# Kernel optimization log

Hardware: AMD Instinct MI355X
Metric: run time of the kernel (lower is better)

The kernel has to match this reference:

```python
import jax, jax.numpy as jnp
import numpy as np

N = 38332        # nodes = poi_len - 1 (pinned by fc_layer in_features)
POI_LEN = 38333
CAT_LEN = 400
POI_DIM = 300
CAT_DIM = 100
C = 128          # gcn_channel
L = 5            # gcn_layers
E = 1200000      # edges
NEG = 0.01       # nn.LeakyReLU default slope
GAT_NEG = 0.2    # GATConv attention slope


def _leaky(x, s=NEG):
    return jnp.where(x > 0, x, s * x)


def _gcn_conv(x, W, b, src, dst, ew):
    # PyG GCNConv: self-loops already appended in (src,dst,ew); symmetric norm
    xw = x @ W
    deg = jax.ops.segment_sum(ew, dst, num_segments=N)
    dinv = jnp.where(deg > 0, jax.lax.rsqrt(deg), 0.0)
    norm = dinv[src] * ew * dinv[dst]
    out = jax.ops.segment_sum(xw[src] * norm[:, None], dst, num_segments=N)
    return out + b


def _gat_conv(x, W, a_src, a_dst, b, src, dst):
    # PyG GATConv, 1 head; self-loops already in (src,dst)
    xw = x @ W                      # [N, C]
    al = xw @ a_src                 # [N]
    ar = xw @ a_dst                 # [N]
    e = _leaky(al[src] + ar[dst], GAT_NEG)          # [E+N]
    emax = jax.ops.segment_max(e, dst, num_segments=N)
    ex = jnp.exp(e - emax[dst])
    denom = jax.ops.segment_sum(ex, dst, num_segments=N)
    att = ex / denom[dst]
    out = jax.ops.segment_sum(xw[src] * att[:, None], dst, num_segments=N)
    return out + b


def _graph_norm(x, gamma, beta, alpha, eps=1e-5):
    # PyG GraphNorm over the single graph (all nodes)
    mean = x.mean(0)
    xc = x - alpha * mean
    var = (xc * xc).mean(0)
    return gamma * xc * jax.lax.rsqrt(var + eps) + beta


def _forward(poi_ids, cat_ids, feat3, edge_index, edge_weight, poi_emb, cat_emb,
             Win, b_in, gcn_W, gcn_b, gn_gamma, gn_beta, gn_alpha,
             gat_W, gat_asrc, gat_adst, gat_b, Wout, b_out,
             fc_W1, fc_b1, fc_W2, fc_b2):
    loops = jnp.arange(N, dtype=edge_index.dtype)
    src = jnp.concatenate([edge_index[0], loops])
    dst = jnp.concatenate([edge_index[1], loops])
    ew = jnp.concatenate([edge_weight, jnp.ones((N,), edge_weight.dtype)])
    # node features: [poi_emb | cat_emb | 3 raw floats] -> [N, 403]
    feat = jnp.concatenate([poi_emb[poi_ids], cat_emb[cat_ids], feat3], axis=1)
    x = _leaky(_gcn_conv(feat, Win, b_in, src, dst, ew))
    for l in range(L):  # GcnUnit stack (shared GraphNorm within a unit)
        t = _leaky(_graph_norm(_gcn_conv(x, gcn_W[l], gcn_b[l], src, dst, ew),
                               gn_gamma[l], gn_beta[l], gn_alpha[l]))
        x = x + t
        t = _leaky(_graph_norm(_gat_conv(x, gat_W[l], gat_asrc[l], gat_adst[l], gat_b[l], src, dst),
                               gn_gamma[l], gn_beta[l], gn_alpha[l]))
        x = x + t
    x = _leaky(_gcn_conv(x, Wout, b_out, src, dst, ew)).reshape(-1)  # [N]
    h = jax.nn.relu(x @ fc_W1 + fc_b1)
    return jax.nn.relu(h @ fc_W2 + fc_b2)  # [POI_LEN]


def setup_inputs() -> dict:
    key = jax.random.key(0)
    ks = iter(jax.random.split(key, 24))
    nrm = lambda s, sc=0.05: jax.random.normal(next(ks), s, dtype=jnp.float32) * sc
    return {
        'poi_ids': jax.random.randint(next(ks), (N,), 0, POI_LEN),
        'cat_ids': jax.random.randint(next(ks), (N,), 0, CAT_LEN),
        'feat3': jax.random.normal(next(ks), (N, 3), dtype=jnp.float32),
        'edge_index': jax.random.randint(next(ks), (2, E), 0, N),
        'edge_weight': jax.random.uniform(next(ks), (E,), dtype=jnp.float32),
        'poi_emb': nrm((POI_LEN, POI_DIM)),
        'cat_emb': nrm((CAT_LEN, CAT_DIM)),
        'Win': nrm((POI_DIM + CAT_DIM + 3, C)),
        'b_in': jnp.zeros((C,), jnp.float32),
        'gcn_W': nrm((L, C, C)),
        'gcn_b': jnp.zeros((L, C), jnp.float32),
        'gn_gamma': jnp.ones((L, C), jnp.float32),
        'gn_beta': jnp.zeros((L, C), jnp.float32),
        'gn_alpha': jnp.ones((L, C), jnp.float32),
        'gat_W': nrm((L, C, C)),
        'gat_asrc': nrm((L, C)),
        'gat_adst': nrm((L, C)),
        'gat_b': jnp.zeros((L, C), jnp.float32),
        'Wout': nrm((C, 1)),
        'b_out': jnp.zeros((1,), jnp.float32),
        'fc_W1': nrm((N, 128)),
        'fc_b1': jnp.zeros((128,), jnp.float32),
        'fc_W2': nrm((128, POI_LEN)),
        'fc_b2': jnp.zeros((POI_LEN,), jnp.float32),
    }


def reference(poi_ids, cat_ids, feat3, edge_index, edge_weight, poi_emb, cat_emb,
              Win, b_in, gcn_W, gcn_b, gn_gamma, gn_beta, gn_alpha,
              gat_W, gat_asrc, gat_adst, gat_b, Wout, b_out,
              fc_W1, fc_b1, fc_W2, fc_b2):
    return _forward(poi_ids, cat_ids, feat3, edge_index, edge_weight, poi_emb, cat_emb,
                    Win, b_in, gcn_W, gcn_b, gn_gamma, gn_beta, gn_alpha,
                    gat_W, gat_asrc, gat_adst, gat_b, Wout, b_out,
                    fc_W1, fc_b1, fc_W2, fc_b2)
```

## Files before the change

kernel.cpp:

```cpp
#include <hip/hip_runtime.h>

typedef unsigned short ushort_t;
typedef __attribute__((ext_vector_type(8))) short short8v;
typedef __attribute__((ext_vector_type(4))) float floatx4;

__device__ __forceinline__ float b2f(ushort_t u) {
    unsigned int x = ((unsigned int)u) << 16;
    float f; __builtin_memcpy(&f, &x, 4); return f;
}
__device__ __forceinline__ ushort_t f2b(float f) {
    unsigned int x; __builtin_memcpy(&x, &f, 4);
    unsigned int lsb = (x >> 16) & 1u;
    x += 0x7fffu + lsb;
    return (ushort_t)(x >> 16);
}
__device__ __forceinline__ float leaky01(float v) { return v > 0.f ? v : 0.01f * v; }

__global__ void init_k(int* cnt, int N) {
    int i = blockIdx.x * 256 + threadIdx.x;
    if (i < N) cnt[i] = 1;
}

__global__ void count_k(const int* __restrict__ ei, int* cnt, int* pos, int E) {
    int e = blockIdx.x * 256 + threadIdx.x;
    if (e < E) pos[e] = atomicAdd(&cnt[ei[E + e]], 1);
}

__launch_bounds__(1024)
__global__ void scan_k(const int* __restrict__ cnt, int* rp, int n) {
    __shared__ int wsum[16];
    int tid = threadIdx.x; int lane = tid & 63, wid = tid >> 6;
    int base = 0;
    for (int start = 0; start < n; start += 4096) {
        int v[4]; int s = 0;
        #pragma unroll
        for (int j = 0; j < 4; ++j) {
            int i = start + tid * 4 + j;
            v[j] = (i < n) ? cnt[i] : 0; s += v[j];
        }
        int sc = s;
        #pragma unroll
        for (int off = 1; off < 64; off <<= 1) {
            int t = __shfl_up(sc, off);
            if (lane >= off) sc += t;
        }
        if (lane == 63) wsum[wid] = sc;
        __syncthreads();
        if (wid == 0) {
            int ws = (lane < 16) ? wsum[lane] : 0;
            #pragma unroll
            for (int off = 1; off < 16; off <<= 1) {
                int t = __shfl_up(ws, off);
                if (lane >= off) ws += t;
            }
            if (lane < 16) wsum[lane] = ws;
        }
        __syncthreads();
        int wbase = (wid > 0) ? wsum[wid - 1] : 0;
        int excl = base + wbase + (sc - s);
        #pragma unroll
        for (int j = 0; j < 4; ++j) {
            int i = start + tid * 4 + j;
            if (i < n) rp[i] = excl;
            excl += v[j];
        }
        int total = wsum[15];
        __syncthreads();
        base += total;
    }
    if (tid == 0) rp[n] = base;
}

__global__ void post_k(const int* __restrict__ rp, float2* er, int N) {
    int i = blockIdx.x * 256 + threadIdx.x;
    if (i < N) er[rp[i]] = make_float2(__int_as_float(i), 1.0f);
}

__global__ void scat_k(const int* __restrict__ ei, const float* __restrict__ ew,
                       const int* __restrict__ rp, const int* __restrict__ pos,
                       float2* er, int E) {
    int e = blockIdx.x * 256 + threadIdx.x;
    if (e < E) {
        int dst = ei[E + e];
        er[rp[dst] + pos[e]] = make_float2(__int_as_float(ei[e]), ew[e]);
    }
}

__global__ void deg_k(const int* __restrict__ rp, const float2* __restrict__ er,
                      float* dinv, int N) {
    int wave = threadIdx.x >> 6, lane = threadIdx.x & 63;
    int node = blockIdx.x * 4 + wave;
    if (node >= N) return;
    int s0 = rp[node], end = rp[node + 1];
    float sum = 0.f;
    for (int s = s0 + lane; s < end; s += 64) sum += er[s].y;
    #pragma unroll
    for (int off = 32; off; off >>= 1) sum += __shfl_xor(sum, off);
    if (lane == 0) dinv[node] = rsqrtf(sum);
}

__global__ void coef_k(const int* __restrict__ rp, float2* er,
                       const float* __restrict__ dinv, int N) {
    int wave = threadIdx.x >> 6, lane = threadIdx.x & 63;
    int node = blockIdx.x * 4 + wave;
    if (node >= N) return;
    int s0 = rp[node], end = rp[node + 1];
    float dn = dinv[node];
    for (int s = s0 + lane; s < end; s += 64) {
        float2 r = er[s];
        int src = __float_as_int(r.x);
        r.y = dinv[src] * r.y * dn;
        er[s] = r;
    }
}

__global__ void prep_w(const float* __restrict__ gcn_W, const float* __restrict__ gat_W,
                       const float* __restrict__ Win, ushort_t* __restrict__ wt,
                       ushort_t* __restrict__ wtin) {
    int idx = blockIdx.x * 256 + threadIdx.x;
    if (idx < 10 * 16384) {
        int l = idx >> 14, r = idx & 16383;
        int n = r >> 7, k = r & 127;
        const float* src = (l < 5) ? (gcn_W + l * 16384) : (gat_W + (l - 5) * 16384);
        wt[idx] = f2b(src[k * 128 + n]);
    } else {
        int idx2 = idx - 10 * 16384;
        if (idx2 < 128 * 320) {
            int n = idx2 / 320, k = idx2 - n * 320;
            wtin[idx2] = f2b(k < 300 ? Win[k * 128 + n] : 0.f);
        }
    }
}

__global__ void cat_proj_k(const float* __restrict__ ce, const float* __restrict__ Win,
                           float* __restrict__ cp) {
    __shared__ float row[100];
    int r = blockIdx.x, tid = threadIdx.x;
    if (tid < 100) row[tid] = ce[r * 100 + tid];
    __syncthreads();
    float acc = 0.f;
    #pragma unroll 4
    for (int k = 0; k < 100; ++k) acc += row[k] * Win[(300 + k) * 128 + tid];
    cp[r * 128 + tid] = acc;
}

__launch_bounds__(256)
__global__ void poi_gemm(const float* __restrict__ pe, const ushort_t* __restrict__ wtin,
                         ushort_t* __restrict__ pp, int P) {
    __shared__ __align__(16) ushort_t As[64 * 328];
    int tid = threadIdx.x;
    int wid = tid >> 6, lane = tid & 63;
    int r0 = blockIdx.x * 64;
    #pragma unroll
    for (int p = 0; p < 19; ++p) {
        int idx = tid + p * 256;
        if (idx < 4800) {
            int row = idx / 75, kq = idx - row * 75;
            int grow = r0 + row;
            float4 v = make_float4(0.f, 0.f, 0.f, 0.f);
            if (grow < P) v = *(const float4*)&pe[(size_t)grow * 300 + kq * 4];
            ushort4 b;
            b.x = f2b(v.x); b.y = f2b(v.y); b.z = f2b(v.z); b.w = f2b(v.w);
            *(ushort4*)&As[row * 328 + kq * 4] = b;
        }
    }
    #pragma unroll
    for (int p = 0; p < 5; ++p) {
        int idx = tid + p * 256;
        if (idx < 1280) {
            int row = idx / 20, j = idx - row * 20;
            As[row * 328 + 300 + j] = 0;
        }
    }
    __syncthreads();
    int m = lane & 15, q = lane >> 4;
    short8v af[10];
    #pragma unroll
    for (int kc = 0; kc < 10; ++kc)
        af[kc] = *(const short8v*)&As[(wid * 16 + m) * 328 + kc * 32 + q * 8];
    #pragma unroll
    for (int ct = 0; ct < 8; ++ct) {
        const ushort_t* wr = wtin + (size_t)(ct * 16 + m) * 320 + q * 8;
        floatx4 acc = {0.f, 0.f, 0.f, 0.f};
        #pragma unroll
        for (int kc = 0; kc < 10; ++kc) {
            short8v b = *(const short8v*)(wr + kc * 32);
            acc = __builtin_amdgcn_mfma_f32_16x16x32_bf16(af[kc], b, acc, 0, 0, 0);
        }
        int col = ct * 16 + m;
        #pragma unroll
        for (int rg = 0; rg < 4; ++rg) {
            int row = r0 + wid * 16 + q * 4 + rg;
            if (row < P) pp[(size_t)row * 128 + col] = f2b(acc[rg]);
        }
    }
}

template <int NORM, int ALAR>
__launch_bounds__(256)
__global__ void gemm_fused(float* __restrict__ x, const float* __restrict__ gsrc,
                           const float* __restrict__ mom,
                           const float* __restrict__ gamma, const float* __restrict__ beta,
                           const float* __restrict__ alpha,
                           const ushort_t* __restrict__ wt,
                           const float* __restrict__ asrc, const float* __restrict__ adst,
                           ushort_t* __restrict__ xw,
                           float* __restrict__ al, float* __restrict__ ar, int N) {
    __shared__ __align__(16) ushort_t As[64 * 136];
    __shared__ float sc[128], sh[128];
    int tid = threadIdx.x;
    if (NORM) {
        if (tid < 128) {
            float mmean = mom[tid] / (float)N;
            float a = alpha[tid];
            float var = mom[128 + tid] / (float)N - 2.f * a * mmean * mmean + a * a * mmean * mmean;
            float s = gamma[tid] * rsqrtf(var + 1e-5f);
            sc[tid] = s;
            sh[tid] = beta[tid] - s * a * mmean;
        }
        __syncthreads();
    }
    int r0 = blockIdx.x * 64;
    #pragma unroll
    for (int p = 0; p < 8; ++p) {
        int idx = tid + p * 256;
        int row = idx >> 5, c4 = (idx & 31) * 4;
        int grow = r0 + row;
        float4 xv = make_float4(0.f, 0.f, 0.f, 0.f);
        if (grow < N) {
            xv = *(const float4*)&x[(size_t)grow * 128 + c4];
            if (NORM) {
                float4 gv = *(const float4*)&gsrc[(size_t)grow * 128 + c4];
                xv.x += leaky01(sc[c4] * gv.x + sh[c4]);
                xv.y += leaky01(sc[c4 + 1] * gv.y + sh[c4 + 1]);
                xv.z += leaky01(sc[c4 + 2] * gv.z + sh[c4 + 2]);
                xv.w += leaky01(sc[c4 + 3] * gv.w + sh[c4 + 3]);
                *(float4*)&x[(size_t)grow * 128 + c4] = xv;
            }
        }
        ushort4 b;
        b.x = f2b(xv.x); b.y = f2b(xv.y); b.z = f2b(xv.z); b.w = f2b(xv.w);
        *(ushort4*)&As[row * 136 + c4] = b;
    }
    __syncthreads();
    int wid = tid >> 6, lane = tid & 63;
    int m = lane & 15, q = lane >> 4;
    const int arr = (wid * 16 + m) * 136 + q * 8;
    short8v a0 = *(const short8v*)&As[arr];
    short8v a1 = *(const short8v*)&As[arr + 32];
    short8v a2 = *(const short8v*)&As[arr + 64];
    short8v a3 = *(const short8v*)&As[arr + 96];
    float alsum[4] = {0.f, 0.f, 0.f, 0.f}, arsum[4] = {0.f, 0.f, 0.f, 0.f};
    #pragma unroll
    for (int ct = 0; ct < 8; ++ct) {
        const ushort_t* wr = wt + (size_t)(ct * 16 + m) * 128 + q * 8;
        short8v b0 = *(const short8v*)(wr);
        short8v b1 = *(const short8v*)(wr + 32);
        short8v b2 = *(const short8v*)(wr + 64);
        short8v b3 = *(const short8v*)(wr + 96);
        floatx4 acc = {0.f, 0.f, 0.f, 0.f};
        acc = __builtin_amdgcn_mfma_f32_16x16x32_bf16(a0, b0, acc, 0, 0, 0);
        acc = __builtin_amdgcn_mfma_f32_16x16x32_bf16(a1, b1, acc, 0, 0, 0);
        acc = __builtin_amdgcn_mfma_f32_16x16x32_bf16(a2, b2, acc, 0, 0, 0);
        acc = __builtin_amdgcn_mfma_f32_16x16x32_bf16(a3, b3, acc, 0, 0, 0);
        int col = ct * 16 + m;
        if (ALAR) {
            float av = asrc[col], dv = adst[col];
            #pragma unroll
            for (int rg = 0; rg < 4; ++rg) {
                alsum[rg] += acc[rg] * av;
                arsum[rg] += acc[rg] * dv;
            }
        }
        #pragma unroll
        for (int rg = 0; rg < 4; ++rg) {
            int row = r0 + wid * 16 + q * 4 + rg;
            if (row < N) xw[(size_t)row * 128 + col] = f2b(acc[rg]);
        }
    }
    if (ALAR) {
        #pragma unroll
        for (int rg = 0; rg < 4; ++rg) {
            #pragma unroll
            for (int off = 1; off < 16; off <<= 1) {
                alsum[rg] += __shfl_xor(alsum[rg], off);
                arsum[rg] += __shfl_xor(arsum[rg], off);
            }
        }
        if (m == 0) {
            #pragma unroll
            for (int rg = 0; rg < 4; ++rg) {
                int row = r0 + wid * 16 + q * 4 + rg;
                if (row < N) { al[row] = alsum[rg]; ar[row] = arsum[rg]; }
            }
        }
    }
}

__global__ void combine_k(const ushort_t* __restrict__ pp, const float* __restrict__ cp,
                          const int* __restrict__ poi_ids, const int* __restrict__ cat_ids,
                          const float* __restrict__ feat3, const float* __restrict__ Win,
                          ushort_t* __restrict__ xw, int N) {
    __shared__ float wf0[128], wf1[128], wf2[128];
    int tid = threadIdx.x;
    if (tid < 128) {
        wf0[tid] = Win[400 * 128 + tid];
        wf1[tid] = Win[401 * 128 + tid];
        wf2[tid] = Win[402 * 128 + tid];
    }
    __syncthreads();
    int node = blockIdx.x * 2 + (tid >> 7);
    int c = tid & 127;
    if (node >= N) return;
    int pid = poi_ids[node], cid = cat_ids[node];
    float f0 = feat3[node * 3], f1 = feat3[node * 3 + 1], f2 = feat3[node * 3 + 2];
    float v = b2f(pp[(size_t)pid * 128 + c]) + cp[cid * 128 + c]
            + f0 * wf0[c] + f1 * wf1[c] + f2 * wf2[c];
    xw[(size_t)node * 128 + c] = f2b(v);
}

template <int MODE>
__launch_bounds__(256)
__global__ void agg_k(const ushort_t* __restrict__ xw, const int* __restrict__ rp,
                      const float2* __restrict__ er,
                      const float* __restrict__ al, const float* __restrict__ ar,
                      const float* __restrict__ bias, float* __restrict__ g, int N) {
    int wave = threadIdx.x >> 6, lane = threadIdx.x & 63;
    int node = blockIdx.x * 4 + wave;
    if (node >= N) return;
    int s0 = __builtin_amdgcn_readfirstlane(rp[node]);
    int end = __builtin_amdgcn_readfirstlane(rp[node + 1]);
    int g8 = lane >> 4;
    int c8 = (lane & 15) * 8;
    float mmax = 0.f, inv = 0.f, ari = 0.f;
    if (MODE == 2) {
        ari = ar[node];
        float mm = -1e30f, ds = 0.f;
        for (int s = s0 + lane; s < end; s += 64) {
            int src = __float_as_int(er[s].x);
            float e = al[src] + ari; e = e > 0.f ? e : 0.2f * e;
            if (e > mm) { ds = ds * __expf(mm - e) + 1.f; mm = e; }
            else ds += __expf(e - mm);
        }
        #pragma unroll
        for (int off = 32; off; off >>= 1) {
            float mo = __shfl_xor(mm, off);
            float dso = __shfl_xor(ds, off);
            float mn = fmaxf(mm, mo);
            ds = ds * __expf(mm - mn) + dso * __expf(mo - mn);
            mm = mn;
        }
        mmax = mm;
        inv = 1.f / ds;
    }
    float acc[8] = {0.f, 0.f, 0.f, 0.f, 0.f, 0.f, 0.f, 0.f};
    auto body = [&](int e) {
        float2 r = er[e];
        int src = __float_as_int(r.x);
        float cf;
        if (MODE == 2) {
            float ev = al[src] + ari; ev = ev > 0.f ? ev : 0.2f * ev;
            cf = __expf(ev - mmax) * inv;
        } else {
            cf = r.y;
        }
        const short8v u = *(const short8v*)&xw[(size_t)src * 128 + c8];
        #pragma unroll
        for (int k = 0; k < 8; ++k) acc[k] += cf * b2f((ushort_t)u[k]);
    };
    int e = s0 + g8;
    for (; e + 28 < end; e += 32) {
        body(e);      body(e + 4);  body(e + 8);  body(e + 12);
        body(e + 16); body(e + 20); body(e + 24); body(e + 28);
    }
    for (; e + 12 < end; e += 16) {
        body(e); body(e + 4); body(e + 8); body(e + 12);
    }
    for (; e < end; e += 4) body(e);
    #pragma unroll
    for (int k = 0; k < 8; ++k) {
        acc[k] += __shfl_xor(acc[k], 16);
        acc[k] += __shfl_xor(acc[k], 32);
    }
    if (g8 == 0) {
        float4 o1, o2;
        o1.x = acc[0] + bias[c8];     o1.y = acc[1] + bias[c8 + 1];
        o1.z = acc[2] + bias[c8 + 2]; o1.w = acc[3] + bias[c8 + 3];
        o2.x = acc[4] + bias[c8 + 4]; o2.y = acc[5] + bias[c8 + 5];
        o2.z = acc[6] + bias[c8 + 6]; o2.w = acc[7] + bias[c8 + 7];
        if (MODE == 1) {
            o1.x = leaky01(o1.x); o1.y = leaky01(o1.y); o1.z = leaky01(o1.z); o1.w = leaky01(o1.w);
            o2.x = leaky01(o2.x); o2.y = leaky01(o2.y); o2.z = leaky01(o2.z); o2.w = leaky01(o2.w);
        }
        *(float4*)&g[(size_t)node * 128 + c8] = o1;
        *(float4*)&g[(size_t)node * 128 + c8 + 4] = o2;
    }
}

__global__ void moments_k(const float* __restrict__ g, float* mom, int n32) {
    __shared__ float s1s[256][4], s2s[256][4];
    int tid = threadIdx.x;
    long long T = (long long)gridDim.x * 256;
    float a1[4] = {0.f, 0.f, 0.f, 0.f}, a2[4] = {0.f, 0.f, 0.f, 0.f};
    const float4* g4 = (const float4*)g;
    for (long long idx = (long long)blockIdx.x * 256 + tid; idx < n32; idx += T) {
        float4 v = g4[idx];
        a1[0] += v.x; a2[0] += v.x * v.x;
        a1[1] += v.y; a2[1] += v.y * v.y;
        a1[2] += v.z; a2[2] += v.z * v.z;
        a1[3] += v.w; a2[3] += v.w * v.w;
    }
    #pragma unroll
    for (int j = 0; j < 4; ++j) { s1s[tid][j] = a1[j]; s2s[tid][j] = a2[j]; }
    __syncthreads();
    if (tid < 32) {
        float r1[4] = {0.f, 0.f, 0.f, 0.f}, r2[4] = {0.f, 0.f, 0.f, 0.f};
        for (int t = tid; t < 256; t += 32) {
            #pragma unroll
            for (int j = 0; j < 4; ++j) { r1[j] += s1s[t][j]; r2[j] += s2s[t][j]; }
        }
        #pragma unroll
        for (int j = 0; j < 4; ++j) {
            atomicAdd(&mom[4 * tid + j], r1[j]);
            atomicAdd(&mom[128 + 4 * tid + j], r2[j]);
        }
    }
}

__global__ void norm_ydot_k(const float* __restrict__ x, const float* __restrict__ g,
                            const float* __restrict__ mom,
                            const float* __restrict__ gamma, const float* __restrict__ beta,
                            const float* __restrict__ alpha, const float* __restrict__ Wout,
                            float* __restrict__ yv, int N) {
    __shared__ float sc[128], sh[128], wv[128];
    int tid = threadIdx.x;
    if (tid < 128) {
        float m = mom[tid] / (float)N;
        float a = alpha[tid];
        float var = mom[128 + tid] / (float)N - 2.f * a * m * m + a * a * m * m;
        float s = gamma[tid] * rsqrtf(var + 1e-5f);
        sc[tid] = s;
        sh[tid] = beta[tid] - s * a * m;
        wv[tid] = Wout[tid];
    }
    __syncthreads();
    int wave = tid >> 6, lane = tid & 63;
    int node = blockIdx.x * 4 + wave;
    if (node >= N) return;
    int c = lane * 2;
    float2 gv = *(const float2*)&g[(size_t)node * 128 + c];
    float2 xv = *(const float2*)&x[(size_t)node * 128 + c];
    float v0 = xv.x + leaky01(sc[c] * gv.x + sh[c]);
    float v1 = xv.y + leaky01(sc[c + 1] * gv.y + sh[c + 1]);
    float acc = v0 * wv[c] + v1 * wv[c + 1];
    #pragma unroll
    for (int off = 32; off; off >>= 1) acc += __shfl_xor(acc, off);
    if (lane == 0) yv[node] = acc;
}

__global__ void aggs_k(const float* __restrict__ yv, const int* __restrict__ rp,
                       const float2* __restrict__ er,
                       const float* __restrict__ b_out, float* xs, int N) {
    int wave = threadIdx.x >> 6, lane = threadIdx.x & 63;
    int node = blockIdx.x * 4 + wave;
    if (node >= N) return;
    int s0 = rp[node], end = rp[node + 1];
    float acc = 0.f;
    for (int s = s0 + lane; s < end; s += 64) {
        float2 r = er[s];
        acc += r.y * yv[__float_as_int(r.x)];
    }
    #pragma unroll
    for (int off = 32; off; off >>= 1) acc += __shfl_xor(acc, off);
    if (lane == 0) xs[node] = leaky01(acc + b_out[0]);
}

__global__ void fc1_k(const float* __restrict__ xs, const float* __restrict__ W1,
                      float* hacc, int N) {
    __shared__ float sd[256];
    int tid = threadIdx.x;
    int j = tid & 127, half = tid >> 7;
    int r0 = blockIdx.x * 256;
    float acc = 0.f;
    for (int rr = half; rr < 256; rr += 2) {
        int r = r0 + rr;
        if (r < N) acc += xs[r] * W1[(size_t)r * 128 + j];
    }
    sd[tid] = acc;
    __syncthreads();
    if (tid < 128) atomicAdd(&hacc[tid], sd[tid] + sd[tid + 128]);
}

__global__ void fc2_k(const float* __restrict__ hacc, const float* __restrict__ b1,
                      const float* __restrict__ W2, const float* __restrict__ b2v,
                      float* out, int P) {
    __shared__ float hs[128];
    int tid = threadIdx.x;
    if (tid < 128) {
        float h = hacc[tid] + b1[tid];
        hs[tid] = h > 0.f ? h : 0.f;
    }
    __syncthreads();
    int p = blockIdx.x * 256 + tid;
    if (p >= P) return;
    float acc = 0.f;
    #pragma unroll 8
    for (int j = 0; j < 128; ++j) acc += hs[j] * W2[(size_t)j * P + p];
    acc += b2v[p];
    out[p] = acc > 0.f ? acc : 0.f;
}

extern "C" void kernel_launch(void* const* d_in, const int* in_sizes, int n_in,
                              void* d_out, int out_size, void* d_ws, size_t ws_size,
                              hipStream_t stream) {
    const int*   poi_ids  = (const int*)d_in[0];
    const int*   cat_ids  = (const int*)d_in[1];
    const float* feat3    = (const float*)d_in[2];
    const int*   ei       = (const int*)d_in[3];
    const float* ew       = (const float*)d_in[4];
    const float* poi_emb  = (const float*)d_in[5];
    const float* cat_emb  = (const float*)d_in[6];
    const float* Win      = (const float*)d_in[7];
    const float* b_in     = (const float*)d_in[8];
    const float* gcn_W    = (const float*)d_in[9];
    const float* gcn_b    = (const float*)d_in[10];
    const float* gn_gamma = (const float*)d_in[11];
    const float* gn_beta  = (const float*)d_in[12];
    const float* gn_alpha = (const float*)d_in[13];
    const float* gat_W    = (const float*)d_in[14];
    const float* gat_asrc = (const float*)d_in[15];
    const float* gat_adst = (const float*)d_in[16];
    const float* gat_b    = (const float*)d_in[17];
    const float* Wout     = (const float*)d_in[18];
    const float* b_out    = (const float*)d_in[19];
    const float* fc_W1    = (const float*)d_in[20];
    const float* fc_b1    = (const float*)d_in[21];
    const float* fc_W2    = (const float*)d_in[22];
    const float* fc_b2    = (const float*)d_in[23];

    const int N = in_sizes[0];
    const int E = in_sizes[4];
    const int POI = in_sizes[5] / 300;
    const int P = out_size;
    const int TOT = E + N;
    const int n128 = N * 128;
    const int n32 = n128 / 4;
    const int NPAD = ((N + 63) / 64) * 64;
    const int PPAD = ((POI + 63) / 64) * 64;

    char* w = (char*)d_ws;
    size_t off = 0;
    auto take = [&](size_t bytes) -> char* {
        char* p = w + off;
        off = (off + bytes + 255) & ~(size_t)255;
        return p;
    };
    float*    x    = (float*)take((size_t)n128 * 4);
    float*    g    = (float*)take((size_t)n128 * 4);
    ushort_t* xw   = (ushort_t*)take((size_t)NPAD * 128 * 2);
    ushort_t* pp   = (ushort_t*)take((size_t)PPAD * 128 * 2);
    float*    cp   = (float*)take((size_t)400 * 128 * 4);
    ushort_t* wt   = (ushort_t*)take((size_t)10 * 16384 * 2);
    ushort_t* wtin = (ushort_t*)take((size_t)128 * 320 * 2);
    int*    rp   = (int*)take((size_t)(N + 1) * 4);
    int*    cnt  = (int*)take((size_t)N * 4);
    int*    pos  = (int*)take((size_t)E * 4);
    float*  dinv = (float*)take((size_t)N * 4);
    float2* er   = (float2*)take((size_t)TOT * 8);
    float*  al   = (float*)take((size_t)N * 4);
    float*  ar   = (float*)take((size_t)N * 4);
    float*  yv   = (float*)take((size_t)N * 4);
    float*  xs   = (float*)take((size_t)N * 4);
    float*  mom  = (float*)take((size_t)(10 * 256 + 128) * 4);
    float*  hacc = mom + 10 * 256;

    const int gN   = (N + 255) / 256;
    const int gE   = (E + 255) / 256;
    const int gMM  = NPAD / 64;
    const int gPOI = PPAD / 64;
    const int gW   = (N + 3) / 4;
    const int gP   = (P + 255) / 256;

    hipMemsetAsync(mom, 0, (size_t)(10 * 256 + 128) * 4, stream);

    init_k<<<gN, 256, 0, stream>>>(cnt, N);
    count_k<<<gE, 256, 0, stream>>>(ei, cnt, pos, E);
    scan_k<<<1, 1024, 0, stream>>>(cnt, rp, N);
    post_k<<<gN, 256, 0, stream>>>(rp, er, N);
    scat_k<<<gE, 256, 0, stream>>>(ei, ew, rp, pos, er, E);
    deg_k<<<gW, 256, 0, stream>>>(rp, er, dinv, N);
    coef_k<<<gW, 256, 0, stream>>>(rp, er, dinv, N);

    prep_w<<<(10 * 16384 + 128 * 320 + 255) / 256, 256, 0, stream>>>(gcn_W, gat_W, Win, wt, wtin);
    cat_proj_k<<<400, 128, 0, stream>>>(cat_emb, Win, cp);
    poi_gemm<<<gPOI, 256, 0, stream>>>(poi_emb, wtin, pp, POI);
    combine_k<<<(N + 1) / 2, 256, 0, stream>>>(pp, cp, poi_ids, cat_ids, feat3, Win, xw, N);
    agg_k<1><<<gW, 256, 0, stream>>>(xw, rp, er, nullptr, nullptr, b_in, x, N);

    for (int l = 0; l < 5; ++l) {
        if (l == 0)
            gemm_fused<0, 0><<<gMM, 256, 0, stream>>>(x, nullptr, nullptr, nullptr, nullptr,
                                                      nullptr, wt, nullptr, nullptr,
                                                      xw, nullptr, nullptr, N);
        else
            gemm_fused<1, 0><<<gMM, 256, 0, stream>>>(x, g, mom + (2 * l - 1) * 256,
                                                      gn_gamma + (l - 1) * 128,
                                                      gn_beta + (l - 1) * 128,
                                                      gn_alpha + (l - 1) * 128,
                                                      wt + (size_t)l * 16384, nullptr, nullptr,
                                                      xw, nullptr, nullptr, N);
        agg_k<0><<<gW, 256, 0, stream>>>(xw, rp, er, nullptr, nullptr, gcn_b + l * 128, g, N);
        moments_k<<<240, 256, 0, stream>>>(g, mom + (2 * l) * 256, n32);

        gemm_fused<1, 1><<<gMM, 256, 0, stream>>>(x, g, mom + (2 * l) * 256,
                                                  gn_gamma + l * 128, gn_beta + l * 128,
                                                  gn_alpha + l * 128,
                                                  wt + (size_t)(5 + l) * 16384,
                                                  gat_asrc + l * 128, gat_adst + l * 128,
                                                  xw, al, ar, N);
        agg_k<2><<<gW, 256, 0, stream>>>(xw, rp, er, al, ar, gat_b + l * 128, g, N);
        moments_k<<<240, 256, 0, stream>>>(g, mom + (2 * l + 1) * 256, n32);
    }

    norm_ydot_k<<<gW, 256, 0, stream>>>(x, g, mom + 9 * 256, gn_gamma + 4 * 128,
                                        gn_beta + 4 * 128, gn_alpha + 4 * 128, Wout, yv, N);
    aggs_k<<<gW, 256, 0, stream>>>(yv, rp, er, b_out, xs, N);

    fc1_k<<<(N + 255) / 256, 256, 0, stream>>>(xs, fc_W1, hacc, N);
    fc2_k<<<gP, 256, 0, stream>>>(hacc, fc_b1, fc_W2, fc_b2, (float*)d_out, P);
}
```

Baseline: 1.563 ms.

## Store node features, aggregates and edge records in packed bf16 format

The residual state x and the aggregation output g move from fp32 to bf16. Each edge record is packed into 32 bits, holding a 16-bit source index and a bf16 coefficient. This halves memory traffic in the gemm, aggregation, moments and norm kernels, and halves the size of the edge array being gathered. In exchange it loses precision in the residual accumulation and the edge weights, and source indices are truncated to 16 bits even though N is 38332. That fits, but only just.

```diff
diff --git a/kernel.cpp b/kernel.cpp
--- a/kernel.cpp
+++ b/kernel.cpp
@@ -1,18 +1,28 @@
 #include <hip/hip_runtime.h>
 
 typedef unsigned short ushort_t;
+typedef unsigned int uint_t;
 typedef __attribute__((ext_vector_type(8))) short short8v;
 typedef __attribute__((ext_vector_type(4))) float floatx4;
 
 __device__ __forceinline__ float b2f(ushort_t u) {
     unsigned int x = ((unsigned int)u) << 16;
     float f; __builtin_memcpy(&f, &x, 4); return f;
+}
+__device__ __forceinline__ float lo16f(uint_t v) {
+    unsigned int x = v << 16; float f; __builtin_memcpy(&f, &x, 4); return f;
+}
+__device__ __forceinline__ float hi16f(uint_t v) {
+    unsigned int x = v & 0xffff0000u; float f; __builtin_memcpy(&f, &x, 4); return f;
 }
 __device__ __forceinline__ ushort_t f2b(float f) {
     unsigned int x; __builtin_memcpy(&x, &f, 4);
     unsigned int lsb = (x >> 16) & 1u;
     x += 0x7fffu + lsb;
     return (ushort_t)(x >> 16);
+}
+__device__ __forceinline__ uint_t pack2(float a, float b) {
+    return (uint_t)f2b(a) | ((uint_t)f2b(b) << 16);
 }
 __device__ __forceinline__ float leaky01(float v) { return v > 0.f ? v : 0.01f * v; }
 
@@ -71,35 +81,35 @@
     if (tid == 0) rp[n] = base;
 }
 
-__global__ void post_k(const int* __restrict__ rp, float2* er, int N) {
+__global__ void post_k(const int* __restrict__ rp, uint_t* er, int N) {
     int i = blockIdx.x * 256 + threadIdx.x;
-    if (i < N) er[rp[i]] = make_float2(__int_as_float(i), 1.0f);
+    if (i < N) er[rp[i]] = (uint_t)i | (0x3F80u << 16);
 }
 
 __global__ void scat_k(const int* __restrict__ ei, const float* __restrict__ ew,
                        const int* __restrict__ rp, const int* __restrict__ pos,
-                       float2* er, int E) {
+                       uint_t* er, int E) {
     int e = blockIdx.x * 256 + threadIdx.x;
     if (e < E) {
         int dst = ei[E + e];
-        er[rp[dst] + pos[e]] = make_float2(__int_as_float(ei[e]), ew[e]);
-    }
-}
-
-__global__ void deg_k(const int* __restrict__ rp, const float2* __restrict__ er,
+        er[rp[dst] + pos[e]] = (uint_t)(ei[e] & 0xffff) | ((uint_t)f2b(ew[e]) << 16);
+    }
+}
+
+__global__ void deg_k(const int* __restrict__ rp, const uint_t* __restrict__ er,
                       float* dinv, int N) {
     int wave = threadIdx.x >> 6, lane = threadIdx.x & 63;
     int node = blockIdx.x * 4 + wave;
     if (node >= N) return;
     int s0 = rp[node], end = rp[node + 1];
     float sum = 0.f;
-    for (int s = s0 + lane; s < end; s += 64) sum += er[s].y;
+    for (int s = s0 + lane; s < end; s += 64) sum += hi16f(er[s]);
     #pragma unroll
     for (int off = 32; off; off >>= 1) sum += __shfl_xor(sum, off);
     if (lane == 0) dinv[node] = rsqrtf(sum);
 }
 
-__global__ void coef_k(const int* __restrict__ rp, float2* er,
+__global__ void coef_k(const int* __restrict__ rp, uint_t* er,
                        const float* __restrict__ dinv, int N) {
     int wave = threadIdx.x >> 6, lane = threadIdx.x & 63;
     int node = blockIdx.x * 4 + wave;
@@ -107,10 +117,10 @@
     int s0 = rp[node], end = rp[node + 1];
     float dn = dinv[node];
     for (int s = s0 + lane; s < end; s += 64) {
-        float2 r = er[s];
-        int src = __float_as_int(r.x);
-        r.y = dinv[src] * r.y * dn;
-        er[s] = r;
+        uint_t r = er[s];
+        int src = r & 0xffffu;
+        float cf = dinv[src] * hi16f(r) * dn;
+        er[s] = (uint_t)src | ((uint_t)f2b(cf) << 16);
     }
 }
 
@@ -198,7 +208,7 @@
 
 template <int NORM, int ALAR>
 __launch_bounds__(256)
-__global__ void gemm_fused(float* __restrict__ x, const float* __restrict__ gsrc,
+__global__ void gemm_fused(ushort_t* __restrict__ xb, const ushort_t* __restrict__ gb,
                            const float* __restrict__ mom,
                            const float* __restrict__ gamma, const float* __restrict__ beta,
                            const float* __restrict__ alpha,
@@ -222,25 +232,29 @@
     }
     int r0 = blockIdx.x * 64;
     #pragma unroll
-    for (int p = 0; p < 8; ++p) {
+    for (int p = 0; p < 4; ++p) {
         int idx = tid + p * 256;
-        int row = idx >> 5, c4 = (idx & 31) * 4;
+        int row = idx >> 4, c8 = (idx & 15) * 8;
         int grow = r0 + row;
-        float4 xv = make_float4(0.f, 0.f, 0.f, 0.f);
+        uint4 xv = make_uint4(0u, 0u, 0u, 0u);
         if (grow < N) {
-            xv = *(const float4*)&x[(size_t)grow * 128 + c4];
+            size_t base = (size_t)grow * 128 + c8;
+            xv = *(const uint4*)&xb[base];
             if (NORM) {
-                float4 gv = *(const float4*)&gsrc[(size_t)grow * 128 + c4];
-                xv.x += leaky01(sc[c4] * gv.x + sh[c4]);
-                xv.y += leaky01(sc[c4 + 1] * gv.y + sh[c4 + 1]);
-                xv.z += leaky01(sc[c4 + 2] * gv.z + sh[c4 + 2]);
-                xv.w += leaky01(sc[c4 + 3] * gv.w + sh[c4 + 3]);
-                *(float4*)&x[(size_t)grow * 128 + c4] = xv;
+                uint4 gv = *(const uint4*)&gb[base];
+                float xf[8] = {lo16f(xv.x), hi16f(xv.x), lo16f(xv.y), hi16f(xv.y),
+                               lo16f(xv.z), hi16f(xv.z), lo16f(xv.w), hi16f(xv.w)};
+                float gf[8] = {lo16f(gv.x), hi16f(gv.x), lo16f(gv.y), hi16f(gv.y),
+                               lo16f(gv.z), hi16f(gv.z), lo16f(gv.w), hi16f(gv.w)};
+                #pragma unroll
+                for (int j = 0; j < 8; ++j)
+                    xf[j] += leaky01(sc[c8 + j] * gf[j] + sh[c8 + j]);
+                xv.x = pack2(xf[0], xf[1]); xv.y = pack2(xf[2], xf[3]);
+                xv.z = pack2(xf[4], xf[5]); xv.w = pack2(xf[6], xf[7]);
+                *(uint4*)&xb[base] = xv;
             }
         }
-        ushort4 b;
-        b.x = f2b(xv.x); b.y = f2b(xv.y); b.z = f2b(xv.z); b.w = f2b(xv.w);
-        *(ushort4*)&As[row * 136 + c4] = b;
+        *(uint4*)&As[row * 136 + c8] = xv;
     }
     __syncthreads();
     int wid = tid >> 6, lane = tid & 63;
@@ -322,9 +336,9 @@
 template <int MODE>
 __launch_bounds__(256)
 __global__ void agg_k(const ushort_t* __restrict__ xw, const int* __restrict__ rp,
-                      const float2* __restrict__ er,
+                      const uint_t* __restrict__ er,
                       const float* __restrict__ al, const float* __restrict__ ar,
-                      const float* __restrict__ bias, float* __restrict__ g, int N) {
+                      const float* __restrict__ bias, ushort_t* __restrict__ gout, int N) {
     int wave = threadIdx.x >> 6, lane = threadIdx.x & 63;
     int node = blockIdx.x * 4 + wave;
     if (node >= N) return;
@@ -337,7 +351,7 @@
         ari = ar[node];
         float mm = -1e30f, ds = 0.f;
         for (int s = s0 + lane; s < end; s += 64) {
-            int src = __float_as_int(er[s].x);
+            int src = er[s] & 0xffffu;
             float e = al[src] + ari; e = e > 0.f ? e : 0.2f * e;
             if (e > mm) { ds = ds * __expf(mm - e) + 1.f; mm = e; }
             else ds += __expf(e - mm);
@@ -355,18 +369,20 @@
     }
     float acc[8] = {0.f, 0.f, 0.f, 0.f, 0.f, 0.f, 0.f, 0.f};
     auto body = [&](int e) {
-        float2 r = er[e];
-        int src = __float_as_int(r.x);
+        uint_t r = er[e];
+        int src = r & 0xffffu;
         float cf;
         if (MODE == 2) {
             float ev = al[src] + ari; ev = ev > 0.f ? ev : 0.2f * ev;
             cf = __expf(ev - mmax) * inv;
         } else {
-            cf = r.y;
-        }
-        const short8v u = *(const short8v*)&xw[(size_t)src * 128 + c8];
-        #pragma unroll
-        for (int k = 0; k < 8; ++k) acc[k] += cf * b2f((ushort_t)u[k]);
+            cf = hi16f(r);
+        }
+        uint4 u = *(const uint4*)&xw[(size_t)src * 128 + c8];
+        acc[0] += cf * lo16f(u.x); acc[1] += cf * hi16f(u.x);
+        acc[2] += cf * lo16f(u.y); acc[3] += cf * hi16f(u.y);
+        acc[4] += cf * lo16f(u.z); acc[5] += cf * hi16f(u.z);
+        acc[6] += cf * lo16f(u.w); acc[7] += cf * hi16f(u.w);
     };
     int e = s0 + g8;
     for (; e + 28 < end; e += 32) {
@@ -383,51 +399,51 @@
         acc[k] += __shfl_xor(acc[k], 32);
     }
     if (g8 == 0) {
-        float4 o1, o2;
-        o1.x = acc[0] + bias[c8];     o1.y = acc[1] + bias[c8 + 1];
-        o1.z = acc[2] + bias[c8 + 2]; o1.w = acc[3] + bias[c8 + 3];
-        o2.x = acc[4] + bias[c8 + 4]; o2.y = acc[5] + bias[c8 + 5];
-        o2.z = acc[6] + bias[c8 + 6]; o2.w = acc[7] + bias[c8 + 7];
-        if (MODE == 1) {
-            o1.x = leaky01(o1.x); o1.y = leaky01(o1.y); o1.z = leaky01(o1.z); o1.w = leaky01(o1.w);
-            o2.x = leaky01(o2.x); o2.y = leaky01(o2.y); o2.z = leaky01(o2.z); o2.w = leaky01(o2.w);
-        }
-        *(float4*)&g[(size_t)node * 128 + c8] = o1;
-        *(float4*)&g[(size_t)node * 128 + c8 + 4] = o2;
-    }
-}
-
-__global__ void moments_k(const float* __restrict__ g, float* mom, int n32) {
-    __shared__ float s1s[256][4], s2s[256][4];
+        float v[8];
+        #pragma unroll
+        for (int k = 0; k < 8; ++k) {
+            v[k] = acc[k] + bias[c8 + k];
+            if (MODE == 1) v[k] = leaky01(v[k]);
+        }
+        uint4 o;
+        o.x = pack2(v[0], v[1]); o.y = pack2(v[2], v[3]);
+        o.z = pack2(v[4], v[5]); o.w = pack2(v[6], v[7]);
+        *(uint4*)&gout[(size_t)node * 128 + c8] = o;
+    }
+}
+
+__global__ void moments_k(const ushort_t* __restrict__ g, float* mom, int n16) {
+    __shared__ float s1s[256][8], s2s[256][8];
     int tid = threadIdx.x;
     long long T = (long long)gridDim.x * 256;
-    float a1[4] = {0.f, 0.f, 0.f, 0.f}, a2[4] = {0.f, 0.f, 0.f, 0.f};
-    const float4* g4 = (const float4*)g;
-    for (long long idx = (long long)blockIdx.x * 256 + tid; idx < n32; idx += T) {
-        float4 v = g4[idx];
-        a1[0] += v.x; a2[0] += v.x * v.x;
-        a1[1] += v.y; a2[1] += v.y * v.y;
-        a1[2] += v.z; a2[2] += v.z * v.z;
-        a1[3] += v.w; a2[3] += v.w * v.w;
-    }
-    #pragma unroll
-    for (int j = 0; j < 4; ++j) { s1s[tid][j] = a1[j]; s2s[tid][j] = a2[j]; }
+    float a1[8] = {0,0,0,0,0,0,0,0}, a2[8] = {0,0,0,0,0,0,0,0};
+    const uint4* g4 = (const uint4*)g;
+    for (long long idx = (long long)blockIdx.x * 256 + tid; idx < n16; idx += T) {
+        uint4 u = g4[idx];
+        float f[8] = {lo16f(u.x), hi16f(u.x), lo16f(u.y), hi16f(u.y),
+                      lo16f(u.z), hi16f(u.z), lo16f(u.w), hi16f(u.w)};
+        #pragma unroll
+        for (int j = 0; j < 8; ++j) { a1[j] += f[j]; a2[j] += f[j] * f[j]; }
+    }
+    #pragma unroll
+    for (int j = 0; j < 8; ++j) { s1s[tid][j] = a1[j]; s2s[tid][j] = a2[j]; }
     __syncthreads();
     if (tid < 32) {
-        float r1[4] = {0.f, 0.f, 0.f, 0.f}, r2[4] = {0.f, 0.f, 0.f, 0.f};
+        float r1[8] = {0,0,0,0,0,0,0,0}, r2[8] = {0,0,0,0,0,0,0,0};
         for (int t = tid; t < 256; t += 32) {
             #pragma unroll
-            for (int j = 0; j < 4; ++j) { r1[j] += s1s[t][j]; r2[j] += s2s[t][j]; }
-        }
-        #pragma unroll
-        for (int j = 0; j < 4; ++j) {
-            atomicAdd(&mom[4 * tid + j], r1[j]);
-            atomicAdd(&mom[128 + 4 * tid + j], r2[j]);
-        }
-    }
-}
-
-__global__ void norm_ydot_k(const float* __restrict__ x, const float* __restrict__ g,
+            for (int j = 0; j < 8; ++j) { r1[j] += s1s[t][j]; r2[j] += s2s[t][j]; }
+        }
+        #pragma unroll
+        for (int j = 0; j < 8; ++j) {
+            int ch = (8 * tid + j) & 127;
+            atomicAdd(&mom[ch], r1[j]);
+            atomicAdd(&mom[128 + ch], r2[j]);
+        }
+    }
+}
+
+__global__ void norm_ydot_k(const ushort_t* __restrict__ xb, const ushort_t* __restrict__ gb,
                             const float* __restrict__ mom,
                             const float* __restrict__ gamma, const float* __restrict__ beta,
                             const float* __restrict__ alpha, const float* __restrict__ Wout,
@@ -448,10 +464,10 @@
     int node = blockIdx.x * 4 + wave;
     if (node >= N) return;
     int c = lane * 2;
-    float2 gv = *(const float2*)&g[(size_t)node * 128 + c];
-    float2 xv = *(const float2*)&x[(size_t)node * 128 + c];
-    float v0 = xv.x + leaky01(sc[c] * gv.x + sh[c]);
-    float v1 = xv.y + leaky01(sc[c + 1] * gv.y + sh[c + 1]);
+    uint_t gv = *(const uint_t*)&gb[(size_t)node * 128 + c];
+    uint_t xv = *(const uint_t*)&xb[(size_t)node * 128 + c];
+    float v0 = lo16f(xv) + leaky01(sc[c] * lo16f(gv) + sh[c]);
+    float v1 = hi16f(xv) + leaky01(sc[c + 1] * hi16f(gv) + sh[c + 1]);
     float acc = v0 * wv[c] + v1 * wv[c + 1];
     #pragma unroll
     for (int off = 32; off; off >>= 1) acc += __shfl_xor(acc, off);
@@ -459,7 +475,7 @@
 }
 
 __global__ void aggs_k(const float* __restrict__ yv, const int* __restrict__ rp,
-                       const float2* __restrict__ er,
+                       const uint_t* __restrict__ er,
                        const float* __restrict__ b_out, float* xs, int N) {
     int wave = threadIdx.x >> 6, lane = threadIdx.x & 63;
     int node = blockIdx.x * 4 + wave;
@@ -467,8 +483,8 @@
     int s0 = rp[node], end = rp[node + 1];
     float acc = 0.f;
     for (int s = s0 + lane; s < end; s += 64) {
-        float2 r = er[s];
-        acc += r.y * yv[__float_as_int(r.x)];
+        uint_t r = er[s];
+        acc += hi16f(r) * yv[r & 0xffffu];
     }
     #pragma unroll
     for (int off = 32; off; off >>= 1) acc += __shfl_xor(acc, off);
@@ -544,7 +560,7 @@
     const int P = out_size;
     const int TOT = E + N;
     const int n128 = N * 128;
-    const int n32 = n128 / 4;
+    const int n16 = n128 / 8;
     const int NPAD = ((N + 63) / 64) * 64;
     const int PPAD = ((POI + 63) / 64) * 64;
 
@@ -555,8 +571,8 @@
         off = (off + bytes + 255) & ~(size_t)255;
         return p;
     };
-    float*    x    = (float*)take((size_t)n128 * 4);
-    float*    g    = (float*)take((size_t)n128 * 4);
+    ushort_t* xb   = (ushort_t*)take((size_t)NPAD * 128 * 2);
+    ushort_t* g    = (ushort_t*)take((size_t)NPAD * 128 * 2);
     ushort_t* xw   = (ushort_t*)take((size_t)NPAD * 128 * 2);
     ushort_t* pp   = (ushort_t*)take((size_t)PPAD * 128 * 2);
     float*    cp   = (float*)take((size_t)400 * 128 * 4);
@@ -566,7 +582,7 @@
     int*    cnt  = (int*)take((size_t)N * 4);
     int*    pos  = (int*)take((size_t)E * 4);
     float*  dinv = (float*)take((size_t)N * 4);
-    float2* er   = (float2*)take((size_t)TOT * 8);
+    uint_t* er   = (uint_t*)take((size_t)TOT * 4);
     float*  al   = (float*)take((size_t)N * 4);
     float*  ar   = (float*)take((size_t)N * 4);
     float*  yv   = (float*)take((size_t)N * 4);
@@ -595,34 +611,34 @@
     cat_proj_k<<<400, 128, 0, stream>>>(cat_emb, Win, cp);
     poi_gemm<<<gPOI, 256, 0, stream>>>(poi_emb, wtin, pp, POI);
     combine_k<<<(N + 1) / 2, 256, 0, stream>>>(pp, cp, poi_ids, cat_ids, feat3, Win, xw, N);
-    agg_k<1><<<gW, 256, 0, stream>>>(xw, rp, er, nullptr, nullptr, b_in, x, N);
+    agg_k<1><<<gW, 256, 0, stream>>>(xw, rp, er, nullptr, nullptr, b_in, xb, N);
 
     for (int l = 0; l < 5; ++l) {
         if (l == 0)
-            gemm_fused<0, 0><<<gMM, 256, 0, stream>>>(x, nullptr, nullptr, nullptr, nullptr,
+            gemm_fused<0, 0><<<gMM, 256, 0, stream>>>(xb, nullptr, nullptr, nullptr, nullptr,
                                                       nullptr, wt, nullptr, nullptr,
                                                       xw, nullptr, nullptr, N);
         else
-            gemm_fused<1, 0><<<gMM, 256, 0, stream>>>(x, g, mom + (2 * l - 1) * 256,
+            gemm_fused<1, 0><<<gMM, 256, 0, stream>>>(xb, g, mom + (2 * l - 1) * 256,
                                                       gn_gamma + (l - 1) * 128,
                                                       gn_beta + (l - 1) * 128,
                                                       gn_alpha + (l - 1) * 128,
                                                       wt + (size_t)l * 16384, nullptr, nullptr,
                                                       xw, nullptr, nullptr, N);
         agg_k<0><<<gW, 256, 0, stream>>>(xw, rp, er, nullptr, nullptr, gcn_b + l * 128, g, N);
-        moments_k<<<240, 256, 0, stream>>>(g, mom + (2 * l) * 256, n32);
-
-        gemm_fused<1, 1><<<gMM, 256, 0, stream>>>(x, g, mom + (2 * l) * 256,
+        moments_k<<<240, 256, 0, stream>>>(g, mom + (2 * l) * 256, n16);
+
+        gemm_fused<1, 1><<<gMM, 256, 0, stream>>>(xb, g, mom + (2 * l) * 256,
                                                   gn_gamma + l * 128, gn_beta + l * 128,
                                                   gn_alpha + l * 128,
                                                   wt + (size_t)(5 + l) * 16384,
                                                   gat_asrc + l * 128, gat_adst + l * 128,
                                                   xw, al, ar, N);
         agg_k<2><<<gW, 256, 0, stream>>>(xw, rp, er, al, ar, gat_b + l * 128, g, N);
-        moments_k<<<240, 256, 0, stream>>>(g, mom + (2 * l + 1) * 256, n32);
-    }
-
-    norm_ydot_k<<<gW, 256, 0, stream>>>(x, g, mom + 9 * 256, gn_gamma + 4 * 128,
+        moments_k<<<240, 256, 0, stream>>>(g, mom + (2 * l + 1) * 256, n16);
+    }
+
+    norm_ydot_k<<<gW, 256, 0, stream>>>(xb, g, mom + 9 * 256, gn_gamma + 4 * 128,
                                         gn_beta + 4 * 128, gn_alpha + 4 * 128, Wout, yv, N);
     aggs_k<<<gW, 256, 0, stream>>>(yv, rp, er, b_out, xs, N);
 
```

New measurement: 2.118 ms. 35.5% more time.
